# Performance work log

Hardware: AMD Instinct MI355X
Metric: run time of the kernel (lower is better)

The kernel has to match this reference:

```python
import jax, jax.numpy as jnp
import numpy as np

EMBED_DIM = 1024
B, S = 4, 2048
SCALE = float(np.sqrt(EMBED_DIM))


def setup_inputs() -> dict:
    key = jax.random.key(0)
    ks = jax.random.split(key, 9)
    d = EMBED_DIM
    init = 1.0 / np.sqrt(d)
    return {
        "query": jax.random.normal(ks[0], (B, S, d), jnp.float32),
        "key": jax.random.normal(ks[1], (B, S, d), jnp.float32),
        "value": jax.random.normal(ks[2], (B, S, d), jnp.float32),
        "wq": jax.random.uniform(ks[3], (d, d), jnp.float32, -init, init),
        "bq": jax.random.uniform(ks[4], (d,), jnp.float32, -init, init),
        "wk": jax.random.uniform(ks[5], (d, d), jnp.float32, -init, init),
        "bk": jax.random.uniform(ks[6], (d,), jnp.float32, -init, init),
        "wv": jax.random.uniform(ks[7], (d, d), jnp.float32, -init, init),
        "bv": jax.random.uniform(ks[8], (d,), jnp.float32, -init, init),
    }


def reference(query, key, value, wq, bq, wk, bk, wv, bv):
    # Linear projections (torch Linear: x @ W^T + b; here weights stored as [in, out])
    q = query @ wq + bq            # [B,S,D]
    k = key @ wk + bk              # [B,S,D]
    v = value @ wv + bv            # [B,S,D]
    scores = jnp.einsum("bqd,bkd->bqk", q, k) / SCALE   # [B,S,S]
    attn = jax.nn.softmax(scores, axis=-1)
    # dropout in eval mode -> identity
    return jnp.einsum("bqk,bkd->bqd", attn, v)          # [B,S,D]
```

## Files before the change

kernel.cpp:

```cpp
#include <hip/hip_runtime.h>
#include <hip/hip_bf16.h>

typedef __attribute__((ext_vector_type(4))) float   f32x4;
typedef __attribute__((ext_vector_type(8))) __bf16  bf16x8;
typedef __attribute__((ext_vector_type(4))) __bf16  bf16x4;

#define NB 4
#define SS 2048
#define DD 1024

__device__ __forceinline__ void gload_lds16(const void* g, void* l) {
  __builtin_amdgcn_global_load_lds((const __attribute__((address_space(1))) void*)g,
                                   (__attribute__((address_space(3))) void*)l,
                                   16, 0, 0);
}

__global__ __launch_bounds__(256) void prep_w_kernel(
    const float* __restrict__ wq, const float* __restrict__ wk, const float* __restrict__ wv,
    const float* __restrict__ bq, const float* __restrict__ bk, const float* __restrict__ bv,
    __bf16* __restrict__ Wt, float* __restrict__ biasbuf)
{
  const int z = blockIdx.z;
  const float* W  = z == 0 ? wq : (z == 1 ? wk : wv);
  const float* bi = z == 0 ? bq : (z == 1 ? bk : bv);
  __bf16* dst = Wt + (size_t)z * (size_t)(DD * DD);
  const int n0 = blockIdx.x * 32, k0 = blockIdx.y * 32;
  __shared__ float t[32][33];
  const int tx = threadIdx.x & 31, ty = threadIdx.x >> 5;
  #pragma unroll
  for (int i = 0; i < 4; i++)
    t[ty + 8 * i][tx] = W[(size_t)(k0 + ty + 8 * i) * DD + n0 + tx];
  __syncthreads();
  #pragma unroll
  for (int i = 0; i < 4; i++)
    dst[(size_t)(n0 + ty + 8 * i) * DD + k0 + tx] = (__bf16)t[tx][ty + 8 * i];
  if (blockIdx.x == 0 && blockIdx.y == 0) {
    #pragma unroll
    for (int i = 0; i < 4; i++)
      biasbuf[z * DD + threadIdx.x + 256 * i] = bi[threadIdx.x + 256 * i];
  }
}


#define A32_OFF(BUF)     ((BUF) * 32768)
#define B2_OFF(BUF, NH)  (65536 + ((BUF)*2 + (NH)) * 16384)

#define DSREAD_B2(DST, BUF, NH)                                                 \
  _Pragma("unroll") for (int ni = 0; ni < 2; ++ni) {                            \
    _Pragma("unroll") for (int ks = 0; ks < 2; ++ks)                            \
      DST[ni][ks] = *(const bf16x8*)(smem + B2_OFF(BUF, NH) + brb2[ks] + ni * 2048); }

#define DSREAD_A32(BUF)                                                         \
  _Pragma("unroll") for (int mi = 0; mi < 4; ++mi) {                            \
    _Pragma("unroll") for (int ks = 0; ks < 2; ++ks) {                          \
      f32x4 u_ = *(const f32x4*)(smem + A32_OFF(BUF) + a32lo[ks] + mi * 4096);  \
      f32x4 v_ = *(const f32x4*)(smem + A32_OFF(BUF) + a32hi[ks] + mi * 4096);  \
      bf16x8 r_;                                                                \
      r_[0]=(__bf16)u_[0]; r_[1]=(__bf16)u_[1]; r_[2]=(__bf16)u_[2]; r_[3]=(__bf16)u_[3]; \
      r_[4]=(__bf16)v_[0]; r_[5]=(__bf16)v_[1]; r_[6]=(__bf16)v_[2]; r_[7]=(__bf16)v_[3]; \
      af[mi][ks] = r_; } }

#define PJ_SA(BUF, T) do { int t_ = (T); if (t_ >= 16) t_ = 0;                  \
  const float* gA_ = Ablk + (size_t)t_ * 64;                                    \
  gload_lds16(gA_ + aof0, smem + A32_OFF(BUF) + tid * 16);                      \
  gload_lds16(gA_ + aof1, smem + A32_OFF(BUF) + 8192 + tid * 16);               \
  gload_lds16(gA_ + aof2, smem + A32_OFF(BUF) + 16384 + tid * 16);              \
  gload_lds16(gA_ + aof3, smem + A32_OFF(BUF) + 24576 + tid * 16);              \
  const __bf16* gB_ = Bblk + (size_t)t_ * 64;                                   \
  gload_lds16(gB_ + boff0, smem + B2_OFF(BUF, 0) + tid * 16);                   \
  gload_lds16(gB_ + boff1, smem + B2_OFF(BUF, 0) + 8192 + tid * 16); } while (0)

#define PJ_SB(BUF, T) do { int t_ = (T); if (t_ >= 16) t_ = 0;                  \
  const __bf16* gB_ = Bblk + (size_t)(128 * 1024) + (size_t)t_ * 64;            \
  gload_lds16(gB_ + boff0, smem + B2_OFF(BUF, 1) + tid * 16);                   \
  gload_lds16(gB_ + boff1, smem + B2_OFF(BUF, 1) + 8192 + tid * 16); } while (0)

#define PJ_MFMA(BF, NH) do {                                                    \
  __builtin_amdgcn_s_barrier();                                                 \
  asm volatile("s_waitcnt lgkmcnt(0)" ::: "memory");                            \
  __builtin_amdgcn_sched_barrier(0);                                            \
  __builtin_amdgcn_s_setprio(1);                                                \
  _Pragma("unroll") for (int mi = 0; mi < 4; ++mi)                              \
  _Pragma("unroll") for (int ni = 0; ni < 2; ++ni)                              \
  _Pragma("unroll") for (int ks = 0; ks < 2; ++ks)                              \
    acc[mi][(NH)*2+ni] = __builtin_amdgcn_mfma_f32_16x16x32_bf16(               \
        af[mi][ks], BF[ni][ks], acc[mi][(NH)*2+ni], 0, 0, 0);                   \
  __builtin_amdgcn_s_setprio(0);                                                \
  __builtin_amdgcn_sched_barrier(0);                                            \
  __builtin_amdgcn_s_barrier(); } while (0)

__global__ __launch_bounds__(512) void proj_kernel(
    const float* __restrict__ Xq, const float* __restrict__ Xk, const float* __restrict__ Xv,
    const __bf16* __restrict__ Wt, const float* __restrict__ bias,
    __bf16* __restrict__ Qo, __bf16* __restrict__ Ko, __bf16* __restrict__ Vt)
{
  extern __shared__ char smem[];

  const int gx = gridDim.x, gy = gridDim.y;
  const int nwg = gx * gy * gridDim.z;
  int lin = blockIdx.x + gx * (blockIdx.y + gy * blockIdx.z);
  const int cpx = nwg >> 3;
  int swz = (lin & 7) * cpx + (lin >> 3);
  const int bx = swz % gx;
  int rem = swz / gx;
  const int by = rem % gy;
  const int bz = rem / gy;

  const long brow = (long)by * 128, bcol = (long)bx * 256;
  const float* Xsel = bz == 0 ? Xq : (bz == 1 ? Xk : Xv);
  const float* Ablk = Xsel + (size_t)brow * 1024;
  const __bf16* Bblk = Wt + (size_t)bz * (DD * DD) + (size_t)bcol * 1024;

  const int tid  = threadIdx.x;
  const int lane = tid & 63;
  const int wid  = tid >> 6;
  const int wm = wid >> 2, wn = wid & 3;
  const int l15 = lane & 15, l4 = lane >> 4;
  const int lx = (lane & 7) << 4;

  int aof0, aof1, aof2, aof3;
  #pragma unroll
  for (int i = 0; i < 4; ++i) {
    const int p = i * 8192 + tid * 16;
    const int r = p >> 8;
    const int kb = (p ^ ((r & 7) << 4)) & 255;
    const int off = r * 1024 + (kb >> 2);
    if (i == 0) aof0 = off; else if (i == 1) aof1 = off;
    else if (i == 2) aof2 = off; else aof3 = off;
  }
  int boff0, boff1;
  #pragma unroll
  for (int i = 0; i < 2; ++i) {
    const int p = i * 8192 + tid * 16;
    const int r = p >> 7;
    const int kb = (p ^ ((r & 7) << 4)) & 127;
    const int off = r * 1024 + (kb >> 1);
    if (i == 0) boff0 = off; else boff1 = off;
  }

  int a32lo[2], a32hi[2];
  #pragma unroll
  for (int ks = 0; ks < 2; ++ks) {
    const int rowb = (wm * 64 + l15) * 256;
    a32lo[ks] = rowb + ((l4 * 32 + ks * 128) ^ lx);
    a32hi[ks] = rowb + ((l4 * 32 + ks * 128 + 16) ^ lx);
  }
  int brb2[2];
  #pragma unroll
  for (int ks = 0; ks < 2; ++ks)
    brb2[ks] = ((((wn * 32 + l15) * 64 + l4 * 8) * 2) + ks * 64) ^ lx;

  f32x4 acc[4][4] = {};
  bf16x8 af[4][2], b0[2][2], b1[2][2];

  PJ_SA(0, 0); PJ_SB(0, 0); PJ_SA(1, 1);
  asm volatile("s_waitcnt vmcnt(6)" ::: "memory");
  __builtin_amdgcn_s_barrier();

  for (int it = 0; it < 8; ++it) {
    const int tt = it * 2;
    PJ_SB(1, tt + 1);
    asm volatile("s_waitcnt vmcnt(10)" ::: "memory");
    DSREAD_A32(0); DSREAD_B2(b0, 0, 0);
    PJ_MFMA(b0, 0);
    PJ_SA(0, tt + 2);
    asm volatile("s_waitcnt vmcnt(14)" ::: "memory");
    DSREAD_B2(b1, 0, 1);
    PJ_MFMA(b1, 1);
    PJ_SB(0, tt + 2);
    asm volatile("s_waitcnt vmcnt(10)" ::: "memory");
    DSREAD_A32(1); DSREAD_B2(b0, 1, 0);
    PJ_MFMA(b0, 0);
    PJ_SA(1, tt + 3);
    asm volatile("s_waitcnt vmcnt(14)" ::: "memory");
    DSREAD_B2(b1, 1, 1);
    PJ_MFMA(b1, 1);
  }

  if (bz == 2) {
    #pragma unroll
    for (int mi = 0; mi < 4; ++mi) {
      #pragma unroll
      for (int n = 0; n < 4; ++n) {
        const long row = brow + wm * 64 + mi * 16 + l4 * 4;
        const long col = bcol + (n >> 1) * 128 + wn * 32 + (n & 1) * 16 + l15;
        const float bvv = bias[2 * DD + col];
        const long bb = row >> 11, s = row & 2047;
        bf16x4 pk = { (__bf16)(acc[mi][n][0] + bvv), (__bf16)(acc[mi][n][1] + bvv),
                      (__bf16)(acc[mi][n][2] + bvv), (__bf16)(acc[mi][n][3] + bvv) };
        *(bf16x4*)&Vt[bb * 2097152 + col * 2048 + s] = pk;
      }
    }
  } else {
    __bf16* C = bz == 0 ? Qo : Ko;
    #pragma unroll
    for (int mi = 0; mi < 4; ++mi) {
      #pragma unroll
      for (int n = 0; n < 4; ++n) {
        const long row = brow + wm * 64 + mi * 16 + l4 * 4;
        const long col = bcol + (n >> 1) * 128 + wn * 32 + (n & 1) * 16 + l15;
        const float bvv = bias[bz * DD + col];
        #pragma unroll
        for (int e = 0; e < 4; ++e)
          C[(row + e) * 1024 + col] = (__bf16)(acc[mi][n][e] + bvv);
      }
    }
  }
}


#define A_OFF(BUF, MH) (((BUF)*2 + (MH)) * 16384)
#define B_OFF(BUF, NH) (65536 + ((BUF)*2 + (NH)) * 16384)

#define STAGE_A(BUF, MH, T) do { int t_ = (T); if (t_ >= NT) t_ = 0;            \
  const __bf16* gs_ = Ablk + (size_t)(MH) * (64 * (size_t)lda) + (size_t)t_ * 64; \
  gload_lds16(gs_ + aoff0, smem + A_OFF(BUF, MH) + tid * 16);                    \
  gload_lds16(gs_ + aoff1, smem + A_OFF(BUF, MH) + 8192 + tid * 16); } while (0)

#define STAGE_B(BUF, NH, T) do { int t_ = (T); if (t_ >= NT) t_ = 0;            \
  const __bf16* gs_ = Bblk + (size_t)(NH) * (32 * (size_t)ldb) + (size_t)t_ * 64; \
  gload_lds16(gs_ + boff0, smem + B_OFF(BUF, NH) + tid * 16);                    \
  gload_lds16(gs_ + boff1, smem + B_OFF(BUF, NH) + 8192 + tid * 16); } while (0)

#define DSREAD_A(DST, BUF, MH)                                                  \
  _Pragma("unroll") for (int mi = 0; mi < 4; ++mi) {                            \
    _Pragma("unroll") for (int ks = 0; ks < 2; ++ks)                            \
      DST[mi][ks] = *(const bf16x8*)(smem + A_OFF(BUF, MH) + arb[ks] + mi * 2048); }

#define DSREAD_BS(DST, BUF, NH)                                                 \
  _Pragma("unroll") for (int ni = 0; ni < 2; ++ni) {                            \
    _Pragma("unroll") for (int ks = 0; ks < 2; ++ks)                            \
      DST[ni][ks] = *(const bf16x8*)(smem + B_OFF(BUF, NH) + brb[ks] + ni * 2048); }

#define BARRIER_MFMA(AF, BF, MH, NH) do {                                       \
  __builtin_amdgcn_s_barrier();                                                 \
  asm volatile("s_waitcnt lgkmcnt(0)" ::: "memory");                            \
  __builtin_amdgcn_sched_barrier(0);                                            \
  __builtin_amdgcn_s_setprio(1);                                                \
  _Pragma("unroll") for (int mi = 0; mi < 4; ++mi)                              \
  _Pragma("unroll") for (int ni = 0; ni < 2; ++ni)                              \
  _Pragma("unroll") for (int ks = 0; ks < 2; ++ks)                              \
    acc[(MH)*4+mi][(NH)*2+ni] = __builtin_amdgcn_mfma_f32_16x16x32_bf16(        \
        AF[mi][ks], BF[ni][ks], acc[(MH)*4+mi][(NH)*2+ni], 0, 0, 0);            \
  __builtin_amdgcn_s_setprio(0);                                                \
  __builtin_amdgcn_sched_barrier(0);                                            \
  __builtin_amdgcn_s_barrier(); } while (0)

__global__ __launch_bounds__(512) void gemm8p_kernel(
    const __bf16* __restrict__ A, const __bf16* __restrict__ B,
    float scale, void* __restrict__ Cout,
    int K, int lda, int ldb, int ldc,
    long strideA, long strideB, long strideC)
{
  extern __shared__ char smem[];

  const int gx = gridDim.x, gy = gridDim.y;
  const int nwg = gx * gy * gridDim.z;
  int lin = blockIdx.x + gx * (blockIdx.y + gy * blockIdx.z);
  const int cpx = nwg >> 3;
  int swz = (lin & 7) * cpx + (lin >> 3);
  const int bx = swz % gx;
  int rem = swz / gx;
  const int by = rem % gy;
  const int bz = rem / gy;

  const long brow = (long)by * 256, bcol = (long)bx * 256;
  const __bf16* Ablk = A + (size_t)bz * strideA + (size_t)brow * lda;
  const __bf16* Bblk = B + (size_t)bz * strideB + (size_t)bcol * ldb;

  const int tid  = threadIdx.x;
  const int lane = tid & 63;
  const int wid  = tid >> 6;
  const int wm = wid >> 2, wn = wid & 3;
  const int l15 = lane & 15, l4 = lane >> 4;
  const int lx = (lane & 7) << 4;

  const int NT = K >> 6;
  const int niter = NT >> 1;

  int aoff0, aoff1, boff0, boff1;
  #pragma unroll
  for (int i = 0; i < 2; ++i) {
    const int p = i * 8192 + tid * 16;
    const int l = p ^ (((p >> 7) & 7) << 4);
    const int r = p >> 7;
    const int kb = l & 127;
    const int av = ((r >> 6) * 128 + (r & 63)) * lda + (kb >> 1);
    const int bv = ((r >> 5) * 64 + (r & 31)) * ldb + (kb >> 1);
    if (i == 0) { aoff0 = av; boff0 = bv; } else { aoff1 = av; boff1 = bv; }
  }

  int arb[2], brb[2];
  #pragma unroll
  for (int ks = 0; ks < 2; ++ks) {
    arb[ks] = ((((wm * 64 + l15) * 64 + l4 * 8) * 2) + ks * 64) ^ lx;
    brb[ks] = ((((wn * 32 + l15) * 64 + l4 * 8) * 2) + ks * 64) ^ lx;
  }

  f32x4 acc[8][4] = {};
  bf16x8 a0[4][2], a1[4][2], b0[2][2], b1[2][2];

  STAGE_B(0, 0, 0); STAGE_A(0, 0, 0); STAGE_A(0, 1, 0); STAGE_B(0, 1, 0);
  STAGE_B(1, 0, 1); STAGE_A(1, 0, 1);
  asm volatile("s_waitcnt vmcnt(4)" ::: "memory");
  __builtin_amdgcn_s_barrier();

  for (int it = 0; it < niter; ++it) {
    const int tt = it * 2;
    DSREAD_A(a0, 0, 0); DSREAD_BS(b0, 0, 0);
    STAGE_A(1, 1, tt + 1);
    BARRIER_MFMA(a0, b0, 0, 0);
    DSREAD_A(a1, 0, 1);
    STAGE_B(1, 1, tt + 1);
    BARRIER_MFMA(a1, b0, 1, 0);
    DSREAD_BS(b1, 0, 1);
    STAGE_B(0, 0, tt + 2);
    BARRIER_MFMA(a0, b1, 0, 1);
    STAGE_A(0, 0, tt + 2);
    asm volatile("s_waitcnt vmcnt(4)" ::: "memory");
    BARRIER_MFMA(a1, b1, 1, 1);
    DSREAD_A(a0, 1, 0); DSREAD_BS(b0, 1, 0);
    STAGE_A(0, 1, tt + 2);
    BARRIER_MFMA(a0, b0, 0, 0);
    DSREAD_A(a1, 1, 1);
    STAGE_B(0, 1, tt + 2);
    BARRIER_MFMA(a1, b0, 1, 0);
    DSREAD_BS(b1, 1, 1);
    STAGE_B(1, 0, tt + 3);
    BARRIER_MFMA(a0, b1, 0, 1);
    STAGE_A(1, 0, tt + 3);
    asm volatile("s_waitcnt vmcnt(4)" ::: "memory");
    BARRIER_MFMA(a1, b1, 1, 1);
  }

  const int cr = l4 * 4;
  __bf16* C = (__bf16*)Cout + (size_t)bz * strideC;
  #pragma unroll
  for (int m = 0; m < 8; ++m) {
    #pragma unroll
    for (int n = 0; n < 4; ++n) {
      const long row = brow + wm * 128 + m * 16 + cr;
      const long col = bcol + wn * 64 + n * 16 + l15;
      #pragma unroll
      for (int e = 0; e < 4; ++e)
        C[(row + e) * (size_t)ldc + col] = (__bf16)__expf(acc[m][n][e] * scale);
    }
  }
}


#define PV_A_OFF(BUF)     ((BUF) * 16384)
#define PV_B_OFF(BUF, NH) (32768 + ((BUF)*2 + (NH)) * 16384)

#define PV_DSA(BUF)                                                             \
  _Pragma("unroll") for (int mi = 0; mi < 4; ++mi) {                            \
    _Pragma("unroll") for (int ks = 0; ks < 2; ++ks)                            \
      af[mi][ks] = *(const bf16x8*)(smem + PV_A_OFF(BUF) + ara[ks] + mi * 2048); }

#define PV_DSB(DST, BUF, NH)                                                    \
  _Pragma("unroll") for (int ni = 0; ni < 2; ++ni) {                            \
    _Pragma("unroll") for (int ks = 0; ks < 2; ++ks)                            \
      DST[ni][ks] = *(const bf16x8*)(smem + PV_B_OFF(BUF, NH) + brb2[ks] + ni * 2048); }

#define PV_SA(BUF, T) do { int t_ = (T); if (t_ >= NT) t_ = 0;                  \
  const __bf16* gA_ = Ablk + (size_t)t_ * 64;                                   \
  gload_lds16(gA_ + aoff0, smem + PV_A_OFF(BUF) + tid * 16);                    \
  gload_lds16(gA_ + aoff1, smem + PV_A_OFF(BUF) + 8192 + tid * 16);             \
  const __bf16* gB_ = Bblk + (size_t)t_ * 64;                                   \
  gload_lds16(gB_ + boff0, smem + PV_B_OFF(BUF, 0) + tid * 16);                 \
  gload_lds16(gB_ + boff1, smem + PV_B_OFF(BUF, 0) + 8192 + tid * 16); } while (0)

#define PV_SB(BUF, T) do { int t_ = (T); if (t_ >= NT) t_ = 0;                  \
  const __bf16* gB_ = Bblk + (size_t)(128 * (size_t)ldb) + (size_t)t_ * 64;     \
  gload_lds16(gB_ + boff0, smem + PV_B_OFF(BUF, 1) + tid * 16);                 \
  gload_lds16(gB_ + boff1, smem + PV_B_OFF(BUF, 1) + 8192 + tid * 16); } while (0)

#define PV_MFMA(BF, NH, DOSUM) do {                                             \
  __builtin_amdgcn_s_barrier();                                                 \
  asm volatile("s_waitcnt lgkmcnt(0)" ::: "memory");                            \
  __builtin_amdgcn_sched_barrier(0);                                            \
  __builtin_amdgcn_s_setprio(1);                                                \
  _Pragma("unroll") for (int mi = 0; mi < 4; ++mi)                              \
  _Pragma("unroll") for (int ni = 0; ni < 2; ++ni)                              \
  _Pragma("unroll") for (int ks = 0; ks < 2; ++ks)                              \
    acc[mi][(NH)*2+ni] = __builtin_amdgcn_mfma_f32_16x16x32_bf16(               \
        af[mi][ks], BF[ni][ks], acc[mi][(NH)*2+ni], 0, 0, 0);                   \
  if (DOSUM) {                                                                  \
    _Pragma("unroll") for (int mi = 0; mi < 4; ++mi)                            \
    _Pragma("unroll") for (int ks = 0; ks < 2; ++ks)                            \
      accs[mi] = __builtin_amdgcn_mfma_f32_16x16x32_bf16(                       \
          af[mi][ks], onesf, accs[mi], 0, 0, 0); }                              \
  __builtin_amdgcn_s_setprio(0);                                                \
  __builtin_amdgcn_sched_barrier(0);                                            \
  __builtin_amdgcn_s_barrier(); } while (0)

__global__ __launch_bounds__(512) void gemm128_kernel(
    const __bf16* __restrict__ A, const __bf16* __restrict__ B,
    void* __restrict__ Cout,
    int K, int lda, int ldb, int ldc,
    long strideA, long strideB, long strideC)
{
  extern __shared__ char smem[];

  const int gx = gridDim.x, gy = gridDim.y;
  const int nwg = gx * gy * gridDim.z;
  int lin = blockIdx.x + gx * (blockIdx.y + gy * blockIdx.z);
  const int cpx = nwg >> 3;
  int swz = (lin & 7) * cpx + (lin >> 3);
  const int bx = swz % gx;
  int rem = swz / gx;
  const int by = rem % gy;
  const int bz = rem / gy;

  const long brow = (long)by * 128, bcol = (long)bx * 256;
  const __bf16* Ablk = A + (size_t)bz * strideA + (size_t)brow * lda;
  const __bf16* Bblk = B + (size_t)bz * strideB + (size_t)bcol * ldb;

  const int tid  = threadIdx.x;
  const int lane = tid & 63;
  const int wid  = tid >> 6;
  const int wm = wid >> 2, wn = wid & 3;
  const int l15 = lane & 15, l4 = lane >> 4;
  const int lx = (lane & 7) << 4;

  const int NT = K >> 6;
  const int niter = NT >> 1;

  int aoff0, aoff1, boff0, boff1;
  #pragma unroll
  for (int i = 0; i < 2; ++i) {
    const int p = i * 8192 + tid * 16;
    const int r = p >> 7;
    const int kb = (p ^ ((r & 7) << 4)) & 127;
    const int av = r * lda + (kb >> 1);
    const int bv = r * ldb + (kb >> 1);
    if (i == 0) { aoff0 = av; boff0 = bv; } else { aoff1 = av; boff1 = bv; }
  }

  int ara[2], brb2[2];
  #pragma unroll
  for (int ks = 0; ks < 2; ++ks) {
    ara[ks]  = ((((wm * 64 + l15) * 64 + l4 * 8) * 2) + ks * 64) ^ lx;
    brb2[ks] = ((((wn * 32 + l15) * 64 + l4 * 8) * 2) + ks * 64) ^ lx;
  }

  f32x4 acc[4][4] = {};
  f32x4 accs[4] = {};
  bf16x8 af[4][2], b0[2][2], b1[2][2];
  bf16x8 onesf;
  #pragma unroll
  for (int j = 0; j < 8; ++j) onesf[j] = (__bf16)1.0f;

  PV_SA(0, 0); PV_SB(0, 0); PV_SA(1, 1);
  asm volatile("s_waitcnt vmcnt(6)" ::: "memory");
  __builtin_amdgcn_s_barrier();

  for (int it = 0; it < niter; ++it) {
    const int tt = it * 2;
    PV_SB(1, tt + 1);
    asm volatile("s_waitcnt vmcnt(6)" ::: "memory");
    PV_DSA(0); PV_DSB(b0, 0, 0);
    PV_MFMA(b0, 0, 1);
    PV_SA(0, tt + 2);
    asm volatile("s_waitcnt vmcnt(6)" ::: "memory");
    PV_DSB(b1, 0, 1);
    PV_MFMA(b1, 1, 0);
    PV_SB(0, tt + 2);
    asm volatile("s_waitcnt vmcnt(6)" ::: "memory");
    PV_DSA(1); PV_DSB(b0, 1, 0);
    PV_MFMA(b0, 0, 1);
    PV_SA(1, tt + 3);
    asm volatile("s_waitcnt vmcnt(6)" ::: "memory");
    PV_DSB(b1, 1, 1);
    PV_MFMA(b1, 1, 0);
  }

  float* C = (float*)Cout + (size_t)bz * strideC;
  #pragma unroll
  for (int mi = 0; mi < 4; ++mi) {
    f32x4 inv;
    #pragma unroll
    for (int e = 0; e < 4; ++e) inv[e] = 1.0f / accs[mi][e];
    #pragma unroll
    for (int n = 0; n < 4; ++n) {
      const long row = brow + wm * 64 + mi * 16 + l4 * 4;
      const long col = bcol + (n >> 1) * 128 + wn * 32 + (n & 1) * 16 + l15;
      #pragma unroll
      for (int e = 0; e < 4; ++e)
        C[(row + e) * (size_t)ldc + col] = acc[mi][n][e] * inv[e];
    }
  }
}

extern "C" void kernel_launch(void* const* d_in, const int* in_sizes, int n_in,
                              void* d_out, int out_size, void* d_ws, size_t ws_size,
                              hipStream_t stream)
{
  const float* query = (const float*)d_in[0];
  const float* key   = (const float*)d_in[1];
  const float* value = (const float*)d_in[2];
  const float* wq = (const float*)d_in[3];
  const float* bq = (const float*)d_in[4];
  const float* wk = (const float*)d_in[5];
  const float* bk = (const float*)d_in[6];
  const float* wv = (const float*)d_in[7];
  const float* bv = (const float*)d_in[8];

  char* ws = (char*)d_ws;
  __bf16* P       = (__bf16*)(ws + 0);
  __bf16* Wt      = (__bf16*)(ws + 33554432);
  float*  biasbuf = (float*)(ws + 39845888);
  __bf16* Qb      = (__bf16*)(ws + 39858176);
  __bf16* Kb      = (__bf16*)(ws + 56635392);
  __bf16* Vt      = (__bf16*)(ws + 73412608);

  hipFuncSetAttribute((const void*)proj_kernel,    hipFuncAttributeMaxDynamicSharedMemorySize, 131072);
  hipFuncSetAttribute((const void*)gemm8p_kernel,  hipFuncAttributeMaxDynamicSharedMemorySize, 131072);
  hipFuncSetAttribute((const void*)gemm128_kernel, hipFuncAttributeMaxDynamicSharedMemorySize, 131072);

  dim3 b256(256), b512(512);

  prep_w_kernel<<<dim3(32, 32, 3), b256, 0, stream>>>(wq, wk, wv, bq, bk, bv, Wt, biasbuf);

  proj_kernel<<<dim3(4, 64, 3), b512, 131072, stream>>>(
      query, key, value, Wt, biasbuf, Qb, Kb, Vt);

  gemm8p_kernel<<<dim3(8, 8, 4), b512, 131072, stream>>>(
      Qb, Kb, 0.03125f, P,
      1024, 1024, 1024, 2048,
      2097152L, 2097152L, 4194304L);

  gemm128_kernel<<<dim3(4, 16, 4), b512, 98304, stream>>>(
      P, Vt, d_out,
      2048, 2048, 2048, 1024,
      4194304L, 2097152L, 2097152L);

  (void)in_sizes; (void)n_in; (void)out_size; (void)ws_size;
}
```

Measured before the change: 173.6 us.

## Convert projection A tiles to bf16 in registers before LDS staging

The projection kernel no longer DMAs fp32 activation tiles straight into LDS and converts them on every LDS read. Each thread now loads the fp32 rows into registers, converts them to bf16 once, and writes the bf16 tile to LDS. The A buffers shrink by half, LDS read traffic per tile drops, and dynamic shared memory falls to 96KB. In exchange the waitcnt schedule is rebuilt around the register loads, which adds VGPR pressure and VALU conversion work inside the pipelined loop.

```diff
diff --git a/kernel.cpp b/kernel.cpp
--- a/kernel.cpp
+++ b/kernel.cpp
@@ -42,38 +42,43 @@
 }
 
 
-#define A32_OFF(BUF)     ((BUF) * 32768)
-#define B2_OFF(BUF, NH)  (65536 + ((BUF)*2 + (NH)) * 16384)
-
-#define DSREAD_B2(DST, BUF, NH)                                                 \
+#define PJ_A_OFF(BUF)     ((BUF) * 16384)
+#define PJ_B_OFF(BUF, NH) (32768 + ((BUF)*2 + (NH)) * 16384)
+
+#define PJ_DSA(BUF)                                                             \
+  _Pragma("unroll") for (int mi = 0; mi < 4; ++mi) {                            \
+    _Pragma("unroll") for (int ks = 0; ks < 2; ++ks)                            \
+      af[mi][ks] = *(const bf16x8*)(smem + PJ_A_OFF(BUF) + ara[ks] + mi * 2048); }
+
+#define PJ_DSB(DST, BUF, NH)                                                    \
   _Pragma("unroll") for (int ni = 0; ni < 2; ++ni) {                            \
     _Pragma("unroll") for (int ks = 0; ks < 2; ++ks)                            \
-      DST[ni][ks] = *(const bf16x8*)(smem + B2_OFF(BUF, NH) + brb2[ks] + ni * 2048); }
-
-#define DSREAD_A32(BUF)                                                         \
-  _Pragma("unroll") for (int mi = 0; mi < 4; ++mi) {                            \
-    _Pragma("unroll") for (int ks = 0; ks < 2; ++ks) {                          \
-      f32x4 u_ = *(const f32x4*)(smem + A32_OFF(BUF) + a32lo[ks] + mi * 4096);  \
-      f32x4 v_ = *(const f32x4*)(smem + A32_OFF(BUF) + a32hi[ks] + mi * 4096);  \
-      bf16x8 r_;                                                                \
-      r_[0]=(__bf16)u_[0]; r_[1]=(__bf16)u_[1]; r_[2]=(__bf16)u_[2]; r_[3]=(__bf16)u_[3]; \
-      r_[4]=(__bf16)v_[0]; r_[5]=(__bf16)v_[1]; r_[6]=(__bf16)v_[2]; r_[7]=(__bf16)v_[3]; \
-      af[mi][ks] = r_; } }
-
-#define PJ_SA(BUF, T) do { int t_ = (T); if (t_ >= 16) t_ = 0;                  \
-  const float* gA_ = Ablk + (size_t)t_ * 64;                                    \
-  gload_lds16(gA_ + aof0, smem + A32_OFF(BUF) + tid * 16);                      \
-  gload_lds16(gA_ + aof1, smem + A32_OFF(BUF) + 8192 + tid * 16);               \
-  gload_lds16(gA_ + aof2, smem + A32_OFF(BUF) + 16384 + tid * 16);              \
-  gload_lds16(gA_ + aof3, smem + A32_OFF(BUF) + 24576 + tid * 16);              \
+      DST[ni][ks] = *(const bf16x8*)(smem + PJ_B_OFF(BUF, NH) + brb2[ks] + ni * 2048); }
+
+#define PJ_GLA(V0, V1, V2, V3, T) do { int t_ = (T); if (t_ >= 16) t_ = 0;      \
+  const float* g_ = Ablk + (size_t)t_ * 64;                                     \
+  V0 = *(const float4*)(g_ + aoffF0); V1 = *(const float4*)(g_ + aoffF0 + 4);   \
+  V2 = *(const float4*)(g_ + aoffF1); V3 = *(const float4*)(g_ + aoffF1 + 4);   \
+  __builtin_amdgcn_sched_barrier(0); } while (0)
+
+#define PJ_WRA(BUF, V0, V1, V2, V3) do {                                        \
+  bf16x8 w0_, w1_;                                                              \
+  w0_[0]=(__bf16)V0.x; w0_[1]=(__bf16)V0.y; w0_[2]=(__bf16)V0.z; w0_[3]=(__bf16)V0.w; \
+  w0_[4]=(__bf16)V1.x; w0_[5]=(__bf16)V1.y; w0_[6]=(__bf16)V1.z; w0_[7]=(__bf16)V1.w; \
+  w1_[0]=(__bf16)V2.x; w1_[1]=(__bf16)V2.y; w1_[2]=(__bf16)V2.z; w1_[3]=(__bf16)V2.w; \
+  w1_[4]=(__bf16)V3.x; w1_[5]=(__bf16)V3.y; w1_[6]=(__bf16)V3.z; w1_[7]=(__bf16)V3.w; \
+  *(bf16x8*)(smem + PJ_A_OFF(BUF) + tid * 16) = w0_;                            \
+  *(bf16x8*)(smem + PJ_A_OFF(BUF) + 8192 + tid * 16) = w1_; } while (0)
+
+#define PJ_SB0(BUF, T) do { int t_ = (T); if (t_ >= 16) t_ = 0;                 \
   const __bf16* gB_ = Bblk + (size_t)t_ * 64;                                   \
-  gload_lds16(gB_ + boff0, smem + B2_OFF(BUF, 0) + tid * 16);                   \
-  gload_lds16(gB_ + boff1, smem + B2_OFF(BUF, 0) + 8192 + tid * 16); } while (0)
-
-#define PJ_SB(BUF, T) do { int t_ = (T); if (t_ >= 16) t_ = 0;                  \
+  gload_lds16(gB_ + boff0, smem + PJ_B_OFF(BUF, 0) + tid * 16);                 \
+  gload_lds16(gB_ + boff1, smem + PJ_B_OFF(BUF, 0) + 8192 + tid * 16); } while (0)
+
+#define PJ_SB1(BUF, T) do { int t_ = (T); if (t_ >= 16) t_ = 0;                 \
   const __bf16* gB_ = Bblk + (size_t)(128 * 1024) + (size_t)t_ * 64;            \
-  gload_lds16(gB_ + boff0, smem + B2_OFF(BUF, 1) + tid * 16);                   \
-  gload_lds16(gB_ + boff1, smem + B2_OFF(BUF, 1) + 8192 + tid * 16); } while (0)
+  gload_lds16(gB_ + boff0, smem + PJ_B_OFF(BUF, 1) + tid * 16);                 \
+  gload_lds16(gB_ + boff1, smem + PJ_B_OFF(BUF, 1) + 8192 + tid * 16); } while (0)
 
 #define PJ_MFMA(BF, NH) do {                                                    \
   __builtin_amdgcn_s_barrier();                                                 \
@@ -118,15 +123,14 @@
   const int l15 = lane & 15, l4 = lane >> 4;
   const int lx = (lane & 7) << 4;
 
-  int aof0, aof1, aof2, aof3;
-  #pragma unroll
-  for (int i = 0; i < 4; ++i) {
+  int aoffF0, aoffF1;
+  #pragma unroll
+  for (int i = 0; i < 2; ++i) {
     const int p = i * 8192 + tid * 16;
-    const int r = p >> 8;
-    const int kb = (p ^ ((r & 7) << 4)) & 255;
-    const int off = r * 1024 + (kb >> 2);
-    if (i == 0) aof0 = off; else if (i == 1) aof1 = off;
-    else if (i == 2) aof2 = off; else aof3 = off;
+    const int r = p >> 7;
+    const int kb = (p ^ ((r & 7) << 4)) & 127;
+    const int aF = r * 1024 + (kb >> 1);
+    if (i == 0) aoffF0 = aF; else aoffF1 = aF;
   }
   int boff0, boff1;
   #pragma unroll
@@ -138,42 +142,47 @@
     if (i == 0) boff0 = off; else boff1 = off;
   }
 
-  int a32lo[2], a32hi[2];
+  int ara[2], brb2[2];
   #pragma unroll
   for (int ks = 0; ks < 2; ++ks) {
-    const int rowb = (wm * 64 + l15) * 256;
-    a32lo[ks] = rowb + ((l4 * 32 + ks * 128) ^ lx);
-    a32hi[ks] = rowb + ((l4 * 32 + ks * 128 + 16) ^ lx);
-  }
-  int brb2[2];
-  #pragma unroll
-  for (int ks = 0; ks < 2; ++ks)
+    ara[ks]  = ((((wm * 64 + l15) * 64 + l4 * 8) * 2) + ks * 64) ^ lx;
     brb2[ks] = ((((wn * 32 + l15) * 64 + l4 * 8) * 2) + ks * 64) ^ lx;
+  }
 
   f32x4 acc[4][4] = {};
   bf16x8 af[4][2], b0[2][2], b1[2][2];
-
-  PJ_SA(0, 0); PJ_SB(0, 0); PJ_SA(1, 1);
+  float4 La0, La1, La2, La3, Lb0, Lb1, Lb2, Lb3;
+
+  PJ_GLA(La0, La1, La2, La3, 0);
+  PJ_GLA(Lb0, Lb1, Lb2, Lb3, 1);
+  PJ_SB0(0, 0); PJ_SB1(0, 0); PJ_SB0(1, 1);
+  asm volatile("s_waitcnt vmcnt(10)" ::: "memory");
+  PJ_WRA(0, La0, La1, La2, La3);
   asm volatile("s_waitcnt vmcnt(6)" ::: "memory");
+  PJ_WRA(1, Lb0, Lb1, Lb2, Lb3);
+  asm volatile("s_waitcnt vmcnt(2) lgkmcnt(0)" ::: "memory");
   __builtin_amdgcn_s_barrier();
 
   for (int it = 0; it < 8; ++it) {
     const int tt = it * 2;
-    PJ_SB(1, tt + 1);
+    PJ_GLA(La0, La1, La2, La3, tt + 2);
+    PJ_SB1(1, tt + 1);
+    PJ_DSA(0); PJ_DSB(b0, 0, 0);
+    PJ_MFMA(b0, 0);
+    PJ_SB0(0, tt + 2);
     asm volatile("s_waitcnt vmcnt(10)" ::: "memory");
-    DSREAD_A32(0); DSREAD_B2(b0, 0, 0);
+    PJ_DSB(b1, 0, 1);
+    PJ_MFMA(b1, 1);
+    asm volatile("s_waitcnt vmcnt(4)" ::: "memory");
+    PJ_WRA(0, La0, La1, La2, La3);
+    PJ_GLA(Lb0, Lb1, Lb2, Lb3, tt + 3);
+    PJ_SB1(0, tt + 2);
+    PJ_DSA(1); PJ_DSB(b0, 1, 0);
     PJ_MFMA(b0, 0);
-    PJ_SA(0, tt + 2);
-    asm volatile("s_waitcnt vmcnt(14)" ::: "memory");
-    DSREAD_B2(b1, 0, 1);
-    PJ_MFMA(b1, 1);
-    PJ_SB(0, tt + 2);
-    asm volatile("s_waitcnt vmcnt(10)" ::: "memory");
-    DSREAD_A32(1); DSREAD_B2(b0, 1, 0);
-    PJ_MFMA(b0, 0);
-    PJ_SA(1, tt + 3);
-    asm volatile("s_waitcnt vmcnt(14)" ::: "memory");
-    DSREAD_B2(b1, 1, 1);
+    PJ_SB0(1, tt + 3);
+    asm volatile("s_waitcnt vmcnt(4)" ::: "memory");
+    PJ_WRA(1, Lb0, Lb1, Lb2, Lb3);
+    PJ_DSB(b1, 1, 1);
     PJ_MFMA(b1, 1);
   }
 
@@ -522,7 +531,7 @@
 
   prep_w_kernel<<<dim3(32, 32, 3), b256, 0, stream>>>(wq, wk, wv, bq, bk, bv, Wt, biasbuf);
 
-  proj_kernel<<<dim3(4, 64, 3), b512, 131072, stream>>>(
+  proj_kernel<<<dim3(4, 64, 3), b512, 98304, stream>>>(
       query, key, value, Wt, biasbuf, Qb, Kb, Vt);
 
   gemm8p_kernel<<<dim3(8, 8, 4), b512, 131072, stream>>>(
```

New measurement: 169.1 us. -2.6%, faster.
